# Kernel tuning notes

Hardware: AMD Instinct MI355X
Metric: run time of the kernel (lower is better)

The kernel has to match this reference:

```python
import jax, jax.numpy as jnp
import numpy as np

D = 64
H_MAX = 64
W_MAX = 64


def setup_inputs() -> dict:
    key = jax.random.key(0)
    k1, k2, k3 = jax.random.split(key, 3)
    q = jax.random.normal(k1, (8, 64, 64, D), dtype=jnp.float32)
    rel_embed_h = jax.random.normal(k2, (2 * H_MAX - 1, D), dtype=jnp.float32) + D ** (-0.5)
    rel_embed_w = jax.random.normal(k3, (2 * W_MAX - 1, D), dtype=jnp.float32) + D ** (-0.5)
    return {"q": q, "rel_embed_h": rel_embed_h, "rel_embed_w": rel_embed_w}


def _rel_to_abs(x):
    """Convert [B, X, Y, 2Y-1] relative logits to [B, X, Y, Y] absolute logits
    via the pad/reshape trick (Bello et al.)."""
    B, X, Y, _ = x.shape
    x = jnp.pad(x, ((0, 0), (0, 0), (0, 0), (0, 1)))        # [B, X, Y, 2Y]
    x = x.reshape(B, X, Y * 2 * Y)                          # flatten last two dims
    x = jnp.pad(x, ((0, 0), (0, 0), (0, Y - 1)))            # [B, X, 2Y^2 + Y - 1]
    x = x.reshape(B, X, Y + 1, 2 * Y - 1)
    return x[:, :, :Y, Y - 1:]                              # [B, X, Y, Y]


def _rel_logits_1d(q, rel_k, perm):
    """Relative logits along the third axis of q ([B, X, Y, d])."""
    B, X, Y, _ = q.shape
    rel = jnp.einsum('bxyd,md->bxym', q, rel_k)             # [B, X, Y, 2Y-1]
    ab = _rel_to_abs(rel)                                   # [B, X, Y, Y]
    ab = jnp.broadcast_to(ab[:, :, None], (B, X, X, Y, Y))  # tile over new axis 2
    return jnp.transpose(ab, perm)


def reference(q, rel_embed_h, rel_embed_w):
    B, H, W, _ = q.shape
    pos_w = _rel_logits_1d(q, rel_embed_w[W_MAX - W:W_MAX + W - 1, :], (0, 1, 3, 2, 4))
    q_t = jnp.transpose(q, (0, 2, 1, 3))                    # [B, W, H, d]
    pos_h = _rel_logits_1d(q_t, rel_embed_h[H_MAX - H:H_MAX + H - 1, :], (0, 3, 1, 4, 2))
    return pos_h + pos_w                                    # [B, H, W, H, W]
```

## Files before the change

### kernel.cpp

```cpp
#include <hip/hip_runtime.h>
#include <hip/hip_bf16.h>


#define D 64
#define SLABS 4

typedef float f32x4 __attribute__((ext_vector_type(4)));

__global__ __launch_bounds__(256) void relpe_kernel(
    const float* __restrict__ q,
    const float* __restrict__ rel_h,
    const float* __restrict__ rel_w,
    float* __restrict__ out) {
    const int base = blockIdx.x * SLABS;
    const int t = threadIdx.x;

    __shared__ __align__(16) float qs[SLABS][D];
    __shared__ __align__(16) float Lh[SLABS][64];
    __shared__ __align__(16) float Lw[SLABS][64];

    qs[t >> 6][t & 63] = q[(size_t)base * D + t];
    __syncthreads();

#pragma unroll
    for (int i = 0; i < 2; ++i) {
        const int id   = t + i * 256;
        const int s    = id >> 7;
        const int j    = id & 63;
        const bool isH = ((id >> 6) & 1) == 0;
        const int sid  = base + s;
        const int w = sid & 63;
        const int h = (sid >> 6) & 63;
        const float* __restrict__ rel =
            isH ? (rel_h + (size_t)(j - h + 63) * D)
                : (rel_w + (size_t)(j - w + 63) * D);
        const float* __restrict__ qv = qs[s];
        float acc = 0.f;
#pragma unroll
        for (int d = 0; d < D; d += 4) {
            const f32x4 r = *reinterpret_cast<const f32x4*>(rel + d);
            acc += qv[d + 0] * r.x;
            acc += qv[d + 1] * r.y;
            acc += qv[d + 2] * r.z;
            acc += qv[d + 3] * r.w;
        }
        if (isH) Lh[s][j] = acc; else Lw[s][j] = acc;
    }
    __syncthreads();

#pragma unroll
    for (int s = 0; s < SLABS; ++s) {
        f32x4* __restrict__ op =
            reinterpret_cast<f32x4*>(out + (size_t)(base + s) * 4096);
        const float* __restrict__ lh = Lh[s];
        const float* __restrict__ lw = Lw[s];
#pragma unroll
        for (int i = 0; i < 4; ++i) {
            const int idx = t + i * 256;
            const int hp  = idx >> 4;
            const int wq  = idx & 15;
            const float a = lh[hp];
            const f32x4 b = *reinterpret_cast<const f32x4*>(&lw[wq * 4]);
            f32x4 v;
            v.x = a + b.x;
            v.y = a + b.y;
            v.z = a + b.z;
            v.w = a + b.w;
            __builtin_nontemporal_store(v, op + idx);
        }
    }
}

extern "C" void kernel_launch(void* const* d_in, const int* in_sizes, int n_in,
                              void* d_out, int out_size, void* d_ws, size_t ws_size,
                              hipStream_t stream) {
    const float* q     = (const float*)d_in[0];
    const float* rel_h = (const float*)d_in[1];
    const float* rel_w = (const float*)d_in[2];
    float* out = (float*)d_out;

    const int nblocks = (8 * 64 * 64) / SLABS;
    relpe_kernel<<<nblocks, 256, 0, stream>>>(q, rel_h, rel_w, out);
}
```

Baseline: 599.9 us.

## Stage relative embeddings in padded LDS and read q via scalar loads

Each block now copies the 64 rel_h rows and 67 rel_w rows it needs into shared memory, padded to a 65-float stride to avoid bank conflicts. The dot products then read embeddings from LDS, and q is read straight from global memory with a wave-uniform slab index so it can go through scalar loads. The dot product is split into four independent accumulators, and the nontemporal output stores are replaced with plain stores. The cost is a much larger shared-memory footprint (about 34 KB per block), which may lower occupancy in a kernel that is dominated by output writes of roughly 537 MB.

New measurement: 559.6 us. 6.7% less time.

```diff
diff --git a/kernel.cpp b/kernel.cpp
--- a/kernel.cpp
+++ b/kernel.cpp
@@ -13,37 +13,51 @@
     const float* __restrict__ rel_w,
     float* __restrict__ out) {
     const int base = blockIdx.x * SLABS;
-    const int t = threadIdx.x;
+    const int w0 = base & 63;
+    const int h  = (base >> 6) & 63;
+    const int t  = threadIdx.x;
 
-    __shared__ __align__(16) float qs[SLABS][D];
+    __shared__ __align__(16) float relh_s[64 * 65];
+    __shared__ __align__(16) float relw_s[67 * 65];
     __shared__ __align__(16) float Lh[SLABS][64];
     __shared__ __align__(16) float Lw[SLABS][64];
 
-    qs[t >> 6][t & 63] = q[(size_t)base * D + t];
+    {
+        const float* __restrict__ srch = rel_h + (63 - h) * D;
+        for (int idx = t; idx < 64 * 16; idx += 256) {
+            const int r = idx >> 4, c = (idx & 15) * 4;
+            const f32x4 v = *reinterpret_cast<const f32x4*>(srch + r * D + c);
+            float* dst = &relh_s[r * 65 + c];
+            dst[0] = v.x; dst[1] = v.y; dst[2] = v.z; dst[3] = v.w;
+        }
+        const float* __restrict__ srcw = rel_w + (60 - w0) * D;
+        for (int idx = t; idx < 67 * 16; idx += 256) {
+            const int r = idx >> 4, c = (idx & 15) * 4;
+            const f32x4 v = *reinterpret_cast<const f32x4*>(srcw + r * D + c);
+            float* dst = &relw_s[r * 65 + c];
+            dst[0] = v.x; dst[1] = v.y; dst[2] = v.z; dst[3] = v.w;
+        }
+    }
     __syncthreads();
 
 #pragma unroll
     for (int i = 0; i < 2; ++i) {
-        const int id   = t + i * 256;
-        const int s    = id >> 7;
-        const int j    = id & 63;
+        const int id = t + i * 256;
+        const int s  = __builtin_amdgcn_readfirstlane((id >> 7) & 3);
         const bool isH = ((id >> 6) & 1) == 0;
-        const int sid  = base + s;
-        const int w = sid & 63;
-        const int h = (sid >> 6) & 63;
-        const float* __restrict__ rel =
-            isH ? (rel_h + (size_t)(j - h + 63) * D)
-                : (rel_w + (size_t)(j - w + 63) * D);
-        const float* __restrict__ qv = qs[s];
-        float acc = 0.f;
+        const int j = id & 63;
+        const float* __restrict__ qg = q + (size_t)(base + s) * D;
+        const float* __restrict__ rl =
+            isH ? &relh_s[j * 65] : &relw_s[(j - s + 3) * 65];
+        float a0 = 0.f, a1 = 0.f, a2 = 0.f, a3 = 0.f;
 #pragma unroll
         for (int d = 0; d < D; d += 4) {
-            const f32x4 r = *reinterpret_cast<const f32x4*>(rel + d);
-            acc += qv[d + 0] * r.x;
-            acc += qv[d + 1] * r.y;
-            acc += qv[d + 2] * r.z;
-            acc += qv[d + 3] * r.w;
+            a0 += qg[d + 0] * rl[d + 0];
+            a1 += qg[d + 1] * rl[d + 1];
+            a2 += qg[d + 2] * rl[d + 2];
+            a3 += qg[d + 3] * rl[d + 3];
         }
+        const float acc = (a0 + a1) + (a2 + a3);
         if (isH) Lh[s][j] = acc; else Lw[s][j] = acc;
     }
     __syncthreads();
@@ -66,7 +80,7 @@
             v.y = a + b.y;
             v.z = a + b.z;
             v.w = a + b.w;
-            __builtin_nontemporal_store(v, op + idx);
+            op[idx] = v;
         }
     }
 }
```
